# Kernel tuning notes

Hardware: AMD Instinct MI355X
Metric: run time of the kernel (lower is better)

The kernel has to match this reference:

```python
import jax, jax.numpy as jnp
import numpy as np

N = 100000   # subcomplex cells (nodes)
E = 600000   # edges in high-adjacency subcomplex graph
NB = 50000   # bridge (rank-0) cells
C = 128      # input_channels
H = 128      # hidden_channels
BN_EPS = 1e-5


def setup_inputs() -> dict:
    key = jax.random.key(0)
    ks = jax.random.split(key, 12)
    x = jax.random.normal(ks[0], (N, C), jnp.float32)
    x0 = jax.random.normal(ks[1], (NB, C), jnp.float32)
    edge_index = jax.random.randint(ks[2], (2, E), 0, N)
    bridge_index = jax.random.randint(ks[3], (E,), 0, NB)
    s1 = 1.0 / np.sqrt(C)
    s2 = 1.0 / np.sqrt(H)
    W1 = jax.random.uniform(ks[4], (C, H), jnp.float32, -s1, s1)
    b1 = jax.random.uniform(ks[5], (H,), jnp.float32, -s1, s1)
    W2 = jax.random.uniform(ks[6], (H, H), jnp.float32, -s2, s2)
    b2 = jax.random.uniform(ks[7], (H,), jnp.float32, -s2, s2)
    gamma1 = jnp.ones((H,), jnp.float32)
    beta1 = jnp.zeros((H,), jnp.float32)
    gamma2 = jnp.ones((H,), jnp.float32)
    beta2 = jnp.zeros((H,), jnp.float32)
    eps_gin = jnp.zeros((), jnp.float32)  # GIN train_eps, init 0
    return {"x": x, "x0": x0, "edge_index": edge_index, "bridge_index": bridge_index,
            "W1": W1, "b1": b1, "gamma1": gamma1, "beta1": beta1,
            "W2": W2, "b2": b2, "gamma2": gamma2, "beta2": beta2,
            "eps_gin": eps_gin}


def _bn(h, gamma, beta):
    # BatchNorm1d in training mode: batch stats over node dim, biased var
    mu = jnp.mean(h, axis=0)
    var = jnp.mean((h - mu) ** 2, axis=0)
    return gamma * (h - mu) * jax.lax.rsqrt(var + BN_EPS) + beta


def reference(x, x0, edge_index, bridge_index, W1, b1, gamma1, beta1,
              W2, b2, gamma2, beta2, eps_gin):
    src, dst = edge_index[0], edge_index[1]
    # edge attributes: gather bridge-cell features per edge  [E, C]
    edge_attr = x0[bridge_index]
    # GINE-style message: relu(x_j + e_ij), scatter-add into destination
    msg = jax.nn.relu(x[src] + edge_attr)
    aggr = jax.ops.segment_sum(msg, dst, num_segments=x.shape[0])  # [N, C]
    h = (1.0 + eps_gin) * x + aggr
    # 2-layer MLP: Linear -> BN -> ReLU, twice
    h = jax.nn.relu(_bn(h @ W1 + b1, gamma1, beta1))
    h = jax.nn.relu(_bn(h @ W2 + b2, gamma2, beta2))
    return h
```

## Files before the change

### kernel.cpp

```cpp
#include <hip/hip_runtime.h>


typedef __attribute__((ext_vector_type(8))) short bf16x8;
typedef __attribute__((ext_vector_type(4))) float floatx4;

__device__ __forceinline__ unsigned short f2bf(float f) {
  unsigned u = __float_as_uint(f);
  u += 0x7fff + ((u >> 16) & 1);
  return (unsigned short)(u >> 16);
}
__device__ __forceinline__ unsigned pk2(float a, float b) {
  return (unsigned)f2bf(a) | ((unsigned)f2bf(b) << 16);
}
__device__ __forceinline__ float bflo(unsigned u) { return __uint_as_float(u << 16); }
__device__ __forceinline__ float bfhi(unsigned u) { return __uint_as_float(u & 0xffff0000u); }

__global__ __launch_bounds__(256) void k_front(
    const float* __restrict__ x, const float* __restrict__ x0,
    const float* __restrict__ W1, const float* __restrict__ W2,
    unsigned short* __restrict__ WT1, unsigned short* __restrict__ WT2,
    uint4* __restrict__ zbase, int zitems, int zblocks,
    uint4* __restrict__ xb, int nx,
    uint4* __restrict__ x0b, int nx0) {
  int b = blockIdx.x;
  int tid = threadIdx.x;
  if (b < 2) {
    const float* W = b ? W2 : W1;
    unsigned short* WT = b ? WT2 : WT1;
#pragma unroll
    for (int i = 0; i < 16; ++i) {
      int g = tid + i * 256;
      int k = g >> 5;
      int n0 = (g & 31) * 4;
      float4 v = *(const float4*)(W + k * 128 + n0);
      WT[(n0 + 0) * 128 + k] = f2bf(v.x);
      WT[(n0 + 1) * 128 + k] = f2bf(v.y);
      WT[(n0 + 2) * 128 + k] = f2bf(v.z);
      WT[(n0 + 3) * 128 + k] = f2bf(v.w);
    }
    return;
  }
  if (b < 2 + zblocks) {
    int t = (b - 2) * 256 + tid;
    if (t < zitems) zbase[t] = make_uint4(0, 0, 0, 0);
    return;
  }
  int t = (b - 2 - zblocks) * 256 + tid;
  const float* s;
  uint4* d;
  if (t < nx) { s = x + (size_t)t * 8; d = xb + t; }
  else {
    t -= nx;
    if (t >= nx0) return;
    s = x0 + (size_t)t * 8; d = x0b + t;
  }
  float4 a = *(const float4*)s;
  float4 c = *(const float4*)(s + 4);
  uint4 o;
  o.x = pk2(a.x, a.y); o.y = pk2(a.z, a.w);
  o.z = pk2(c.x, c.y); o.w = pk2(c.z, c.w);
  *d = o;
}

__global__ __launch_bounds__(256) void k_scatter(
    const int* __restrict__ src, const int* __restrict__ dst,
    const int* __restrict__ bri, int* __restrict__ cnt,
    int2* __restrict__ slots, int E_) {
  int e = blockIdx.x * 256 + threadIdx.x;
  if (e >= E_) return;
  int d = dst[e];
  int pos = atomicAdd(&cnt[d], 1);
  if (pos < 32) slots[d * 32 + pos] = make_int2(src[e], bri[e]);
}

__device__ __forceinline__ void acc8(float* acc, uint4 xa, uint4 ea) {
  acc[0] += fmaxf(bflo(xa.x) + bflo(ea.x), 0.f);
  acc[1] += fmaxf(bfhi(xa.x) + bfhi(ea.x), 0.f);
  acc[2] += fmaxf(bflo(xa.y) + bflo(ea.y), 0.f);
  acc[3] += fmaxf(bfhi(xa.y) + bfhi(ea.y), 0.f);
  acc[4] += fmaxf(bflo(xa.z) + bflo(ea.z), 0.f);
  acc[5] += fmaxf(bfhi(xa.z) + bfhi(ea.z), 0.f);
  acc[6] += fmaxf(bflo(xa.w) + bflo(ea.w), 0.f);
  acc[7] += fmaxf(bfhi(xa.w) + bfhi(ea.w), 0.f);
}

__global__ __launch_bounds__(256) void k_aggr(
    const uint4* __restrict__ xb, const uint4* __restrict__ x0b,
    const int* __restrict__ cnt, const int2* __restrict__ slots,
    const float* __restrict__ eps, uint4* __restrict__ aggr, int n) {
  int tid = threadIdx.x;
  int node = blockIdx.x * 32 + (tid >> 3);
  if (node >= n) return;
  int q = (tid & 7) + blockIdx.y * 8;
  float s = 1.0f + eps[0];
  float acc[8];
  uint4 xi = xb[(size_t)node * 16 + q];
  acc[0] = s * bflo(xi.x); acc[1] = s * bfhi(xi.x);
  acc[2] = s * bflo(xi.y); acc[3] = s * bfhi(xi.y);
  acc[4] = s * bflo(xi.z); acc[5] = s * bfhi(xi.z);
  acc[6] = s * bflo(xi.w); acc[7] = s * bfhi(xi.w);
  int end = cnt[node];
  if (end > 32) end = 32;
  int base = node * 32;
  int j = 0;
  for (; j + 4 <= end; j += 4) {
    int4 pa = *(const int4*)(slots + base + j);
    int4 pb = *(const int4*)(slots + base + j + 2);
    uint4 xa0 = xb[(size_t)pa.x * 16 + q];
    uint4 ea0 = x0b[(size_t)pa.y * 16 + q];
    uint4 xa1 = xb[(size_t)pa.z * 16 + q];
    uint4 ea1 = x0b[(size_t)pa.w * 16 + q];
    uint4 xa2 = xb[(size_t)pb.x * 16 + q];
    uint4 ea2 = x0b[(size_t)pb.y * 16 + q];
    uint4 xa3 = xb[(size_t)pb.z * 16 + q];
    uint4 ea3 = x0b[(size_t)pb.w * 16 + q];
    acc8(acc, xa0, ea0);
    acc8(acc, xa1, ea1);
    acc8(acc, xa2, ea2);
    acc8(acc, xa3, ea3);
  }
  if (j + 2 <= end) {
    int4 pa = *(const int4*)(slots + base + j);
    uint4 xa0 = xb[(size_t)pa.x * 16 + q];
    uint4 ea0 = x0b[(size_t)pa.y * 16 + q];
    uint4 xa1 = xb[(size_t)pa.z * 16 + q];
    uint4 ea1 = x0b[(size_t)pa.w * 16 + q];
    acc8(acc, xa0, ea0);
    acc8(acc, xa1, ea1);
    j += 2;
  }
  if (j < end) {
    int2 p = slots[base + j];
    uint4 xa0 = xb[(size_t)p.x * 16 + q];
    uint4 ea0 = x0b[(size_t)p.y * 16 + q];
    acc8(acc, xa0, ea0);
  }
  uint4 o;
  o.x = pk2(acc[0], acc[1]); o.y = pk2(acc[2], acc[3]);
  o.z = pk2(acc[4], acc[5]); o.w = pk2(acc[6], acc[7]);
  aggr[(size_t)node * 16 + q] = o;
}

__global__ __launch_bounds__(256) void k_gemmb(
    const unsigned short* A, const unsigned short* __restrict__ WT,
    const float* __restrict__ bias,
    const float* __restrict__ psum, const float* __restrict__ psq,
    const float* __restrict__ gam, const float* __restrict__ bet,
    unsigned short* Out,
    float* __restrict__ part,
    int nrows, float inv_n, int fuse) {
  __shared__ unsigned short LDSraw[128 * 144];
  unsigned short* As = LDSraw;
  unsigned short* Bs = LDSraw + 128 * 72;
  __shared__ float sL[128], hL[128];
  __shared__ float redS[4][64], redQ[4][64];
  int tid = threadIdx.x;
  if (fuse && tid < 128) {
    float mu = psum[tid] * inv_n;
    float var = psq[tid] * inv_n - mu * mu;
    float rs = rsqrtf(var + 1e-5f);
    float sc = gam[tid] * rs;
    sL[tid] = sc;
    hL[tid] = bet[tid] - mu * sc;
  }
  __syncthreads();

  int row0 = blockIdx.x * 128;
  int lane = tid & 63;
  int wid = tid >> 6;
  int wr = (wid >> 1) * 64;
  int wc = (wid & 1) * 64;
  int lr = lane & 15;
  int quad = lane >> 4;

  floatx4 acc[4][4];
#pragma unroll
  for (int mi = 0; mi < 4; ++mi)
#pragma unroll
    for (int ni = 0; ni < 4; ++ni) acc[mi][ni] = (floatx4)0.0f;

  for (int kc = 0; kc < 128; kc += 64) {
    if (kc) __syncthreads();
#pragma unroll
    for (int i = 0; i < 4; ++i) {
      int g = tid + i * 256;
      int r = g >> 3;
      int c8 = g & 7;
      int row = row0 + r;
      uint4 v = make_uint4(0, 0, 0, 0);
      if (row < nrows)
        v = *(const uint4*)(A + (size_t)row * 128 + kc + c8 * 8);
      if (fuse) {
        int k = kc + c8 * 8;
        v.x = pk2(fmaxf(fmaf(sL[k + 0], bflo(v.x), hL[k + 0]), 0.f),
                  fmaxf(fmaf(sL[k + 1], bfhi(v.x), hL[k + 1]), 0.f));
        v.y = pk2(fmaxf(fmaf(sL[k + 2], bflo(v.y), hL[k + 2]), 0.f),
                  fmaxf(fmaf(sL[k + 3], bfhi(v.y), hL[k + 3]), 0.f));
        v.z = pk2(fmaxf(fmaf(sL[k + 4], bflo(v.z), hL[k + 4]), 0.f),
                  fmaxf(fmaf(sL[k + 5], bfhi(v.z), hL[k + 5]), 0.f));
        v.w = pk2(fmaxf(fmaf(sL[k + 6], bflo(v.w), hL[k + 6]), 0.f),
                  fmaxf(fmaf(sL[k + 7], bfhi(v.w), hL[k + 7]), 0.f));
      }
      *(uint4*)&As[r * 72 + c8 * 8] = v;
    }
#pragma unroll
    for (int i = 0; i < 4; ++i) {
      int g = tid + i * 256;
      int nn = g >> 3;
      int c8 = g & 7;
      *(uint4*)&Bs[nn * 72 + c8 * 8] =
          *(const uint4*)(WT + (size_t)nn * 128 + kc + c8 * 8);
    }
    __syncthreads();
#pragma unroll
    for (int ks = 0; ks < 2; ++ks) {
      int k0 = ks * 32 + quad * 8;
      bf16x8 af[4], bfr[4];
#pragma unroll
      for (int mi = 0; mi < 4; ++mi)
        af[mi] = *(const bf16x8*)&As[(wr + mi * 16 + lr) * 72 + k0];
#pragma unroll
      for (int ni = 0; ni < 4; ++ni)
        bfr[ni] = *(const bf16x8*)&Bs[(wc + ni * 16 + lr) * 72 + k0];
#pragma unroll
      for (int mi = 0; mi < 4; ++mi)
#pragma unroll
        for (int ni = 0; ni < 4; ++ni)
          acc[mi][ni] = __builtin_amdgcn_mfma_f32_16x16x32_bf16(
              af[mi], bfr[ni], acc[mi][ni], 0, 0, 0);
    }
  }
  __syncthreads();

  float bv[4];
#pragma unroll
  for (int ni = 0; ni < 4; ++ni) bv[ni] = bias[wc + ni * 16 + lr];
  float s_sum[4] = {0.f, 0.f, 0.f, 0.f};
  float s_sq[4]  = {0.f, 0.f, 0.f, 0.f};
#pragma unroll
  for (int mi = 0; mi < 4; ++mi) {
#pragma unroll
    for (int r = 0; r < 4; ++r) {
      int rl = wr + mi * 16 + quad * 4 + r;
      bool ok = (row0 + rl) < nrows;
#pragma unroll
      for (int ni = 0; ni < 4; ++ni) {
        int col = wc + ni * 16 + lr;
        float v = acc[mi][ni][r] + bv[ni];
        LDSraw[rl * 136 + col] = f2bf(v);
        if (ok) { s_sum[ni] += v; s_sq[ni] += v * v; }
      }
    }
  }
#pragma unroll
  for (int ni = 0; ni < 4; ++ni) {
    s_sum[ni] += __shfl_xor(s_sum[ni], 16, 64);
    s_sum[ni] += __shfl_xor(s_sum[ni], 32, 64);
    s_sq[ni]  += __shfl_xor(s_sq[ni], 16, 64);
    s_sq[ni]  += __shfl_xor(s_sq[ni], 32, 64);
  }
  if (quad == 0) {
#pragma unroll
    for (int ni = 0; ni < 4; ++ni) {
      redS[wid][ni * 16 + lr] = s_sum[ni];
      redQ[wid][ni * 16 + lr] = s_sq[ni];
    }
  }
  __syncthreads();
  if (tid < 128) {
    int half = tid >> 6;
    int cl = tid & 63;
    part[(size_t)blockIdx.x * 256 + tid] = redS[half][cl] + redS[half + 2][cl];
    part[(size_t)blockIdx.x * 256 + 128 + tid] = redQ[half][cl] + redQ[half + 2][cl];
  }
#pragma unroll
  for (int i = 0; i < 8; ++i) {
    int g = tid + i * 256;
    int r = g >> 4;
    int c8 = g & 15;
    if (row0 + r < nrows)
      *(uint4*)(Out + (size_t)(row0 + r) * 128 + c8 * 8) =
          *(const uint4*)&LDSraw[r * 136 + c8 * 8];
  }
}

__global__ __launch_bounds__(256) void k_red(
    const float* __restrict__ part, float* __restrict__ dst, int nb) {
  int c = threadIdx.x;
  int r0 = blockIdx.x * 32;
  int r1 = r0 + 32;
  if (r1 > nb) r1 = nb;
  float a = 0.f;
  for (int r = r0; r < r1; ++r) a += part[(size_t)r * 256 + c];
  unsafeAtomicAdd(&dst[c], a);
}

__global__ __launch_bounds__(256) void k_bnrelu(
    const uint4* __restrict__ h, const float* __restrict__ psum,
    const float* __restrict__ psq, const float* __restrict__ gam,
    const float* __restrict__ bet, float* __restrict__ out,
    int items, float inv_n) {
  __shared__ float sL[128], hL[128];
  int tid = threadIdx.x;
  if (tid < 128) {
    float mu = psum[tid] * inv_n;
    float var = psq[tid] * inv_n - mu * mu;
    float rs = rsqrtf(var + 1e-5f);
    float sc = gam[tid] * rs;
    sL[tid] = sc;
    hL[tid] = bet[tid] - mu * sc;
  }
  __syncthreads();
  int t = blockIdx.x * 256 + tid;
  if (t >= items) return;
  int c = (t & 15) * 8;
  uint4 v = h[t];
  float4 o1, o2;
  o1.x = fmaxf(fmaf(sL[c + 0], bflo(v.x), hL[c + 0]), 0.f);
  o1.y = fmaxf(fmaf(sL[c + 1], bfhi(v.x), hL[c + 1]), 0.f);
  o1.z = fmaxf(fmaf(sL[c + 2], bflo(v.y), hL[c + 2]), 0.f);
  o1.w = fmaxf(fmaf(sL[c + 3], bfhi(v.y), hL[c + 3]), 0.f);
  o2.x = fmaxf(fmaf(sL[c + 4], bflo(v.z), hL[c + 4]), 0.f);
  o2.y = fmaxf(fmaf(sL[c + 5], bfhi(v.z), hL[c + 5]), 0.f);
  o2.z = fmaxf(fmaf(sL[c + 6], bflo(v.w), hL[c + 6]), 0.f);
  o2.w = fmaxf(fmaf(sL[c + 7], bfhi(v.w), hL[c + 7]), 0.f);
  ((float4*)out)[(size_t)t * 2 + 0] = o1;
  ((float4*)out)[(size_t)t * 2 + 1] = o2;
}

extern "C" void kernel_launch(void* const* d_in, const int* in_sizes, int n_in,
                              void* d_out, int out_size, void* d_ws, size_t ws_size,
                              hipStream_t stream) {
  const float* x   = (const float*)d_in[0];
  const float* x0  = (const float*)d_in[1];
  const int*   ei  = (const int*)d_in[2];
  const int*   bi  = (const int*)d_in[3];
  const float* W1  = (const float*)d_in[4];
  const float* b1  = (const float*)d_in[5];
  const float* g1  = (const float*)d_in[6];
  const float* be1 = (const float*)d_in[7];
  const float* W2  = (const float*)d_in[8];
  const float* b2  = (const float*)d_in[9];
  const float* g2  = (const float*)d_in[10];
  const float* be2 = (const float*)d_in[11];
  const float* eps = (const float*)d_in[12];

  int N  = in_sizes[0] / 128;
  int NB = in_sizes[1] / 128;
  int E_ = in_sizes[3];
  const int* srcp = ei;
  const int* dstp = ei + E_;

  int2* slots = (int2*)d_ws;
  int* cnt    = (int*)(slots + (size_t)N * 32);
  float* stats = (float*)(cnt + N);
  float* sum1 = stats;
  float* sum2 = stats + 256;
  unsigned short* WT1  = (unsigned short*)(stats + 512);
  unsigned short* WT2  = WT1 + 16384;
  unsigned short* abuf = WT2 + 16384;

  unsigned short* xb  = (unsigned short*)d_out;
  unsigned short* x0b = xb + (size_t)N * 128;
  float* part = (float*)d_out;

  int zitems  = (N + 512 + 3) / 4;
  int zblocks = (zitems + 255) / 256;
  int nx  = N * 16;
  int nx0 = NB * 16;
  int cvtblocks = (nx + nx0 + 255) / 256;
  float inv_n = 1.0f / (float)N;

  k_front<<<2 + zblocks + cvtblocks, 256, 0, stream>>>(
      x, x0, W1, W2, WT1, WT2, (uint4*)cnt, zitems, zblocks,
      (uint4*)xb, nx, (uint4*)x0b, nx0);

  k_scatter<<<(E_ + 255) / 256, 256, 0, stream>>>(srcp, dstp, bi, cnt,
                                                  slots, E_);

  dim3 agrid((N * 8 + 255) / 256, 2);
  k_aggr<<<agrid, 256, 0, stream>>>(
      (const uint4*)xb, (const uint4*)x0b, cnt, slots, eps,
      (uint4*)abuf, N);

  int gblocks = (N + 127) / 128;
  int rblocks = (gblocks + 31) / 32;
  k_gemmb<<<gblocks, 256, 0, stream>>>(abuf, WT1, b1, nullptr, nullptr,
                                       nullptr, nullptr, abuf, part,
                                       N, inv_n, 0);
  k_red<<<rblocks, 256, 0, stream>>>(part, sum1, gblocks);
  k_gemmb<<<gblocks, 256, 0, stream>>>(abuf, WT2, b2, sum1, sum1 + 128,
                                       g1, be1, abuf, part, N, inv_n, 1);
  k_red<<<rblocks, 256, 0, stream>>>(part, sum2, gblocks);

  k_bnrelu<<<(N * 16 + 255) / 256, 256, 0, stream>>>(
      (const uint4*)abuf, sum2, sum2 + 128, g2, be2, (float*)d_out,
      N * 16, inv_n);
}
```

Measured before the change: 294.8 us.

## Fuse neighbor aggregation into first GEMM, building A tiles directly in LDS

The separate aggregation kernel is removed. The first GEMM now computes each 128-row aggregated tile itself, gathering neighbor and edge features into LDS one 64-column K-chunk at a time before running the MFMAs. This removes the write and re-read of the aggregated activation buffer and one kernel launch. The cost is a gather-heavy, latency-bound phase inside the GEMM kernel with fewer concurrent waves per row (only 256 threads per 128 rows, with `unroll 1`), which may hurt memory-level parallelism compared with the standalone aggregation grid. The partial-stats buffer is also moved so it no longer overlaps the bf16 copies of x and x0 that the fused kernel still reads.

```diff
diff --git a/kernel.cpp b/kernel.cpp
--- a/kernel.cpp
+++ b/kernel.cpp
@@ -84,17 +84,12 @@
   acc[7] += fmaxf(bfhi(xa.w) + bfhi(ea.w), 0.f);
 }
 
-__global__ __launch_bounds__(256) void k_aggr(
+__device__ __forceinline__ uint4 aggr_row(
     const uint4* __restrict__ xb, const uint4* __restrict__ x0b,
     const int* __restrict__ cnt, const int2* __restrict__ slots,
-    const float* __restrict__ eps, uint4* __restrict__ aggr, int n) {
-  int tid = threadIdx.x;
-  int node = blockIdx.x * 32 + (tid >> 3);
-  if (node >= n) return;
-  int q = (tid & 7) + blockIdx.y * 8;
-  float s = 1.0f + eps[0];
+    float s, int node, int qq) {
   float acc[8];
-  uint4 xi = xb[(size_t)node * 16 + q];
+  uint4 xi = xb[(size_t)node * 16 + qq];
   acc[0] = s * bflo(xi.x); acc[1] = s * bfhi(xi.x);
   acc[2] = s * bflo(xi.y); acc[3] = s * bfhi(xi.y);
   acc[4] = s * bflo(xi.z); acc[5] = s * bfhi(xi.z);
@@ -106,14 +101,14 @@
   for (; j + 4 <= end; j += 4) {
     int4 pa = *(const int4*)(slots + base + j);
     int4 pb = *(const int4*)(slots + base + j + 2);
-    uint4 xa0 = xb[(size_t)pa.x * 16 + q];
-    uint4 ea0 = x0b[(size_t)pa.y * 16 + q];
-    uint4 xa1 = xb[(size_t)pa.z * 16 + q];
-    uint4 ea1 = x0b[(size_t)pa.w * 16 + q];
-    uint4 xa2 = xb[(size_t)pb.x * 16 + q];
-    uint4 ea2 = x0b[(size_t)pb.y * 16 + q];
-    uint4 xa3 = xb[(size_t)pb.z * 16 + q];
-    uint4 ea3 = x0b[(size_t)pb.w * 16 + q];
+    uint4 xa0 = xb[(size_t)pa.x * 16 + qq];
+    uint4 ea0 = x0b[(size_t)pa.y * 16 + qq];
+    uint4 xa1 = xb[(size_t)pa.z * 16 + qq];
+    uint4 ea1 = x0b[(size_t)pa.w * 16 + qq];
+    uint4 xa2 = xb[(size_t)pb.x * 16 + qq];
+    uint4 ea2 = x0b[(size_t)pb.y * 16 + qq];
+    uint4 xa3 = xb[(size_t)pb.z * 16 + qq];
+    uint4 ea3 = x0b[(size_t)pb.w * 16 + qq];
     acc8(acc, xa0, ea0);
     acc8(acc, xa1, ea1);
     acc8(acc, xa2, ea2);
@@ -121,24 +116,138 @@
   }
   if (j + 2 <= end) {
     int4 pa = *(const int4*)(slots + base + j);
-    uint4 xa0 = xb[(size_t)pa.x * 16 + q];
-    uint4 ea0 = x0b[(size_t)pa.y * 16 + q];
-    uint4 xa1 = xb[(size_t)pa.z * 16 + q];
-    uint4 ea1 = x0b[(size_t)pa.w * 16 + q];
+    uint4 xa0 = xb[(size_t)pa.x * 16 + qq];
+    uint4 ea0 = x0b[(size_t)pa.y * 16 + qq];
+    uint4 xa1 = xb[(size_t)pa.z * 16 + qq];
+    uint4 ea1 = x0b[(size_t)pa.w * 16 + qq];
     acc8(acc, xa0, ea0);
     acc8(acc, xa1, ea1);
     j += 2;
   }
   if (j < end) {
     int2 p = slots[base + j];
-    uint4 xa0 = xb[(size_t)p.x * 16 + q];
-    uint4 ea0 = x0b[(size_t)p.y * 16 + q];
+    uint4 xa0 = xb[(size_t)p.x * 16 + qq];
+    uint4 ea0 = x0b[(size_t)p.y * 16 + qq];
     acc8(acc, xa0, ea0);
   }
   uint4 o;
   o.x = pk2(acc[0], acc[1]); o.y = pk2(acc[2], acc[3]);
   o.z = pk2(acc[4], acc[5]); o.w = pk2(acc[6], acc[7]);
-  aggr[(size_t)node * 16 + q] = o;
+  return o;
+}
+
+__global__ __launch_bounds__(256) void k_agemm(
+    const uint4* __restrict__ xb, const uint4* __restrict__ x0b,
+    const int* __restrict__ cnt, const int2* __restrict__ slots,
+    const float* __restrict__ eps,
+    const unsigned short* __restrict__ WT,
+    const float* __restrict__ bias,
+    unsigned short* __restrict__ Out,
+    float* __restrict__ part,
+    int nrows) {
+  __shared__ unsigned short LDSraw[128 * 144];
+  unsigned short* As = LDSraw;
+  __shared__ float redS[4][64], redQ[4][64];
+  int tid = threadIdx.x;
+  int row0 = blockIdx.x * 128;
+  int lane = tid & 63;
+  int wid = tid >> 6;
+  int wr = (wid >> 1) * 64;
+  int wc = (wid & 1) * 64;
+  int lr = lane & 15;
+  int quad = lane >> 4;
+  float s = 1.0f + eps[0];
+
+  floatx4 acc[4][4];
+#pragma unroll
+  for (int mi = 0; mi < 4; ++mi)
+#pragma unroll
+    for (int ni = 0; ni < 4; ++ni) acc[mi][ni] = (floatx4)0.0f;
+
+  for (int kc = 0; kc < 128; kc += 64) {
+    if (kc) __syncthreads();
+    int qq = (tid & 7) + (kc >> 3);
+#pragma unroll 1
+    for (int it = 0; it < 4; ++it) {
+      int r = it * 32 + (tid >> 3);
+      int node = row0 + r;
+      uint4 v = make_uint4(0, 0, 0, 0);
+      if (node < nrows)
+        v = aggr_row(xb, x0b, cnt, slots, s, node, qq);
+      *(uint4*)&As[r * 72 + (tid & 7) * 8] = v;
+    }
+    __syncthreads();
+#pragma unroll
+    for (int ks = 0; ks < 2; ++ks) {
+      int k0 = ks * 32 + quad * 8;
+      bf16x8 af[4], bfr[4];
+#pragma unroll
+      for (int mi = 0; mi < 4; ++mi)
+        af[mi] = *(const bf16x8*)&As[(wr + mi * 16 + lr) * 72 + k0];
+#pragma unroll
+      for (int ni = 0; ni < 4; ++ni)
+        bfr[ni] = *(const bf16x8*)(WT + (size_t)(wc + ni * 16 + lr) * 128 +
+                                   kc + k0);
+#pragma unroll
+      for (int mi = 0; mi < 4; ++mi)
+#pragma unroll
+        for (int ni = 0; ni < 4; ++ni)
+          acc[mi][ni] = __builtin_amdgcn_mfma_f32_16x16x32_bf16(
+              af[mi], bfr[ni], acc[mi][ni], 0, 0, 0);
+    }
+  }
+  __syncthreads();
+
+  float bv[4];
+#pragma unroll
+  for (int ni = 0; ni < 4; ++ni) bv[ni] = bias[wc + ni * 16 + lr];
+  float s_sum[4] = {0.f, 0.f, 0.f, 0.f};
+  float s_sq[4]  = {0.f, 0.f, 0.f, 0.f};
+#pragma unroll
+  for (int mi = 0; mi < 4; ++mi) {
+#pragma unroll
+    for (int r = 0; r < 4; ++r) {
+      int rl = wr + mi * 16 + quad * 4 + r;
+      bool ok = (row0 + rl) < nrows;
+#pragma unroll
+      for (int ni = 0; ni < 4; ++ni) {
+        int col = wc + ni * 16 + lr;
+        float v = acc[mi][ni][r] + bv[ni];
+        LDSraw[rl * 136 + col] = f2bf(v);
+        if (ok) { s_sum[ni] += v; s_sq[ni] += v * v; }
+      }
+    }
+  }
+#pragma unroll
+  for (int ni = 0; ni < 4; ++ni) {
+    s_sum[ni] += __shfl_xor(s_sum[ni], 16, 64);
+    s_sum[ni] += __shfl_xor(s_sum[ni], 32, 64);
+    s_sq[ni]  += __shfl_xor(s_sq[ni], 16, 64);
+    s_sq[ni]  += __shfl_xor(s_sq[ni], 32, 64);
+  }
+  if (quad == 0) {
+#pragma unroll
+    for (int ni = 0; ni < 4; ++ni) {
+      redS[wid][ni * 16 + lr] = s_sum[ni];
+      redQ[wid][ni * 16 + lr] = s_sq[ni];
+    }
+  }
+  __syncthreads();
+  if (tid < 128) {
+    int half = tid >> 6;
+    int cl = tid & 63;
+    part[(size_t)blockIdx.x * 256 + tid] = redS[half][cl] + redS[half + 2][cl];
+    part[(size_t)blockIdx.x * 256 + 128 + tid] = redQ[half][cl] + redQ[half + 2][cl];
+  }
+#pragma unroll
+  for (int i = 0; i < 8; ++i) {
+    int g = tid + i * 256;
+    int r = g >> 4;
+    int c8 = g & 15;
+    if (row0 + r < nrows)
+      *(uint4*)(Out + (size_t)(row0 + r) * 128 + c8 * 8) =
+          *(const uint4*)&LDSraw[r * 136 + c8 * 8];
+  }
 }
 
 __global__ __launch_bounds__(256) void k_gemmb(
@@ -362,7 +471,7 @@
 
   unsigned short* xb  = (unsigned short*)d_out;
   unsigned short* x0b = xb + (size_t)N * 128;
-  float* part = (float*)d_out;
+  float* part = (float*)((char*)d_out + (size_t)(N + NB) * 256);
 
   int zitems  = (N + 512 + 3) / 4;
   int zblocks = (zitems + 255) / 256;
@@ -378,16 +487,11 @@
   k_scatter<<<(E_ + 255) / 256, 256, 0, stream>>>(srcp, dstp, bi, cnt,
                                                   slots, E_);
 
-  dim3 agrid((N * 8 + 255) / 256, 2);
-  k_aggr<<<agrid, 256, 0, stream>>>(
-      (const uint4*)xb, (const uint4*)x0b, cnt, slots, eps,
-      (uint4*)abuf, N);
-
   int gblocks = (N + 127) / 128;
   int rblocks = (gblocks + 31) / 32;
-  k_gemmb<<<gblocks, 256, 0, stream>>>(abuf, WT1, b1, nullptr, nullptr,
-                                       nullptr, nullptr, abuf, part,
-                                       N, inv_n, 0);
+  k_agemm<<<gblocks, 256, 0, stream>>>(
+      (const uint4*)xb, (const uint4*)x0b, cnt, slots, eps, WT1, b1,
+      abuf, part, N);
   k_red<<<rblocks, 256, 0, stream>>>(part, sum1, gblocks);
   k_gemmb<<<gblocks, 256, 0, stream>>>(abuf, WT2, b2, sum1, sum1 + 128,
                                        g1, be1, abuf, part, N, inv_n, 1);
```

After: 320.7 us. 1.09x slower.

## Merge convert, scatter and aggregate into one cooperative kernel with grid syncs

Applied to the files above, without the earlier changes.

Replaces the three launches (bf16 conversion with zeroing, edge scatter into slots, neighbor aggregation) with a single cooperative kernel. It uses grid-stride loops and grid-wide barriers between phases, and falls back to three per-phase launches if the cooperative launch is unavailable. The goal is to cut kernel launch gaps and tail effects between the preprocessing stages. In exchange, the grid is capped at 2048 blocks, which may lower parallelism in the gather phase, and grid.sync adds barrier cost.

```diff
diff --git a/kernel.cpp b/kernel.cpp
--- a/kernel.cpp
+++ b/kernel.cpp
@@ -1,4 +1,7 @@
 #include <hip/hip_runtime.h>
+#include <hip/hip_cooperative_groups.h>
+
+namespace cg = cooperative_groups;
 
 
 typedef __attribute__((ext_vector_type(8))) short bf16x8;
@@ -15,63 +18,17 @@
 __device__ __forceinline__ float bflo(unsigned u) { return __uint_as_float(u << 16); }
 __device__ __forceinline__ float bfhi(unsigned u) { return __uint_as_float(u & 0xffff0000u); }
 
-__global__ __launch_bounds__(256) void k_front(
-    const float* __restrict__ x, const float* __restrict__ x0,
-    const float* __restrict__ W1, const float* __restrict__ W2,
-    unsigned short* __restrict__ WT1, unsigned short* __restrict__ WT2,
-    uint4* __restrict__ zbase, int zitems, int zblocks,
-    uint4* __restrict__ xb, int nx,
-    uint4* __restrict__ x0b, int nx0) {
-  int b = blockIdx.x;
-  int tid = threadIdx.x;
-  if (b < 2) {
-    const float* W = b ? W2 : W1;
-    unsigned short* WT = b ? WT2 : WT1;
-#pragma unroll
-    for (int i = 0; i < 16; ++i) {
-      int g = tid + i * 256;
-      int k = g >> 5;
-      int n0 = (g & 31) * 4;
-      float4 v = *(const float4*)(W + k * 128 + n0);
-      WT[(n0 + 0) * 128 + k] = f2bf(v.x);
-      WT[(n0 + 1) * 128 + k] = f2bf(v.y);
-      WT[(n0 + 2) * 128 + k] = f2bf(v.z);
-      WT[(n0 + 3) * 128 + k] = f2bf(v.w);
-    }
-    return;
-  }
-  if (b < 2 + zblocks) {
-    int t = (b - 2) * 256 + tid;
-    if (t < zitems) zbase[t] = make_uint4(0, 0, 0, 0);
-    return;
-  }
-  int t = (b - 2 - zblocks) * 256 + tid;
-  const float* s;
-  uint4* d;
-  if (t < nx) { s = x + (size_t)t * 8; d = xb + t; }
-  else {
-    t -= nx;
-    if (t >= nx0) return;
-    s = x0 + (size_t)t * 8; d = x0b + t;
-  }
-  float4 a = *(const float4*)s;
-  float4 c = *(const float4*)(s + 4);
-  uint4 o;
-  o.x = pk2(a.x, a.y); o.y = pk2(a.z, a.w);
-  o.z = pk2(c.x, c.y); o.w = pk2(c.z, c.w);
-  *d = o;
-}
-
-__global__ __launch_bounds__(256) void k_scatter(
-    const int* __restrict__ src, const int* __restrict__ dst,
-    const int* __restrict__ bri, int* __restrict__ cnt,
-    int2* __restrict__ slots, int E_) {
-  int e = blockIdx.x * 256 + threadIdx.x;
-  if (e >= E_) return;
-  int d = dst[e];
-  int pos = atomicAdd(&cnt[d], 1);
-  if (pos < 32) slots[d * 32 + pos] = make_int2(src[e], bri[e]);
-}
+struct PreParams {
+  const float* x; const float* x0;
+  const int* src; const int* dst; const int* bri;
+  const float* eps;
+  int2* slots; int* cnt;
+  const float* W1; const float* W2;
+  unsigned short* WT1; unsigned short* WT2;
+  unsigned short* abuf;
+  float* dout;
+  int N; int NB; int E;
+};
 
 __device__ __forceinline__ void acc8(float* acc, uint4 xa, uint4 ea) {
   acc[0] += fmaxf(bflo(xa.x) + bflo(ea.x), 0.f);
@@ -84,17 +41,12 @@
   acc[7] += fmaxf(bfhi(xa.w) + bfhi(ea.w), 0.f);
 }
 
-__global__ __launch_bounds__(256) void k_aggr(
+__device__ __forceinline__ uint4 aggr_row(
     const uint4* __restrict__ xb, const uint4* __restrict__ x0b,
     const int* __restrict__ cnt, const int2* __restrict__ slots,
-    const float* __restrict__ eps, uint4* __restrict__ aggr, int n) {
-  int tid = threadIdx.x;
-  int node = blockIdx.x * 32 + (tid >> 3);
-  if (node >= n) return;
-  int q = (tid & 7) + blockIdx.y * 8;
-  float s = 1.0f + eps[0];
+    float s, int node, int qq) {
   float acc[8];
-  uint4 xi = xb[(size_t)node * 16 + q];
+  uint4 xi = xb[(size_t)node * 16 + qq];
   acc[0] = s * bflo(xi.x); acc[1] = s * bfhi(xi.x);
   acc[2] = s * bflo(xi.y); acc[3] = s * bfhi(xi.y);
   acc[4] = s * bflo(xi.z); acc[5] = s * bfhi(xi.z);
@@ -106,14 +58,14 @@
   for (; j + 4 <= end; j += 4) {
     int4 pa = *(const int4*)(slots + base + j);
     int4 pb = *(const int4*)(slots + base + j + 2);
-    uint4 xa0 = xb[(size_t)pa.x * 16 + q];
-    uint4 ea0 = x0b[(size_t)pa.y * 16 + q];
-    uint4 xa1 = xb[(size_t)pa.z * 16 + q];
-    uint4 ea1 = x0b[(size_t)pa.w * 16 + q];
-    uint4 xa2 = xb[(size_t)pb.x * 16 + q];
-    uint4 ea2 = x0b[(size_t)pb.y * 16 + q];
-    uint4 xa3 = xb[(size_t)pb.z * 16 + q];
-    uint4 ea3 = x0b[(size_t)pb.w * 16 + q];
+    uint4 xa0 = xb[(size_t)pa.x * 16 + qq];
+    uint4 ea0 = x0b[(size_t)pa.y * 16 + qq];
+    uint4 xa1 = xb[(size_t)pa.z * 16 + qq];
+    uint4 ea1 = x0b[(size_t)pa.w * 16 + qq];
+    uint4 xa2 = xb[(size_t)pb.x * 16 + qq];
+    uint4 ea2 = x0b[(size_t)pb.y * 16 + qq];
+    uint4 xa3 = xb[(size_t)pb.z * 16 + qq];
+    uint4 ea3 = x0b[(size_t)pb.w * 16 + qq];
     acc8(acc, xa0, ea0);
     acc8(acc, xa1, ea1);
     acc8(acc, xa2, ea2);
@@ -121,24 +73,97 @@
   }
   if (j + 2 <= end) {
     int4 pa = *(const int4*)(slots + base + j);
-    uint4 xa0 = xb[(size_t)pa.x * 16 + q];
-    uint4 ea0 = x0b[(size_t)pa.y * 16 + q];
-    uint4 xa1 = xb[(size_t)pa.z * 16 + q];
-    uint4 ea1 = x0b[(size_t)pa.w * 16 + q];
+    uint4 xa0 = xb[(size_t)pa.x * 16 + qq];
+    uint4 ea0 = x0b[(size_t)pa.y * 16 + qq];
+    uint4 xa1 = xb[(size_t)pa.z * 16 + qq];
+    uint4 ea1 = x0b[(size_t)pa.w * 16 + qq];
     acc8(acc, xa0, ea0);
     acc8(acc, xa1, ea1);
     j += 2;
   }
   if (j < end) {
-    int2 p = slots[base + j];
-    uint4 xa0 = xb[(size_t)p.x * 16 + q];
-    uint4 ea0 = x0b[(size_t)p.y * 16 + q];
+    int2 pp = slots[base + j];
+    uint4 xa0 = xb[(size_t)pp.x * 16 + qq];
+    uint4 ea0 = x0b[(size_t)pp.y * 16 + qq];
     acc8(acc, xa0, ea0);
   }
   uint4 o;
   o.x = pk2(acc[0], acc[1]); o.y = pk2(acc[2], acc[3]);
   o.z = pk2(acc[4], acc[5]); o.w = pk2(acc[6], acc[7]);
-  aggr[(size_t)node * 16 + q] = o;
+  return o;
+}
+
+__device__ __forceinline__ void run_pre(const PreParams& p, int phase) {
+  int tid = threadIdx.x;
+  int nb = gridDim.x;
+  int gt0 = blockIdx.x * 256 + tid;
+  int gstride = nb * 256;
+  uint4* xbv  = (uint4*)p.dout;
+  uint4* x0bv = xbv + (size_t)p.N * 16;
+  int nx = p.N * 16, nx0 = p.NB * 16;
+
+  if (phase == 0) {
+    int zitems = (p.N + 512 + 3) >> 2;
+    for (int t = gt0; t < zitems; t += gstride)
+      ((uint4*)p.cnt)[t] = make_uint4(0, 0, 0, 0);
+    for (int t = gt0; t < 8192; t += gstride) {
+      int w = t >> 12;
+      int g = t & 4095;
+      const float* W = w ? p.W2 : p.W1;
+      unsigned short* WT = w ? p.WT2 : p.WT1;
+      int k = g >> 5;
+      int n0 = (g & 31) * 4;
+      float4 v = *(const float4*)(W + k * 128 + n0);
+      WT[(n0 + 0) * 128 + k] = f2bf(v.x);
+      WT[(n0 + 1) * 128 + k] = f2bf(v.y);
+      WT[(n0 + 2) * 128 + k] = f2bf(v.z);
+      WT[(n0 + 3) * 128 + k] = f2bf(v.w);
+    }
+    for (int t = gt0; t < nx + nx0; t += gstride) {
+      const float* sp;
+      uint4* dp;
+      if (t < nx) { sp = p.x + (size_t)t * 8; dp = xbv + t; }
+      else { sp = p.x0 + (size_t)(t - nx) * 8; dp = x0bv + (t - nx); }
+      float4 a = *(const float4*)sp;
+      float4 c4 = *(const float4*)(sp + 4);
+      uint4 o;
+      o.x = pk2(a.x, a.y); o.y = pk2(a.z, a.w);
+      o.z = pk2(c4.x, c4.y); o.w = pk2(c4.z, c4.w);
+      *dp = o;
+    }
+  } else if (phase == 1) {
+    for (int e = gt0; e < p.E; e += gstride) {
+      int d = p.dst[e];
+      int pos = atomicAdd(&p.cnt[d], 1);
+      if (pos < 32) p.slots[d * 32 + pos] = make_int2(p.src[e], p.bri[e]);
+    }
+  } else {
+    float s = 1.0f + p.eps[0];
+    int nAb = (p.N * 8 + 255) / 256;
+    for (int t = blockIdx.x; t < 2 * nAb; t += nb) {
+      int by = (t >= nAb) ? 1 : 0;
+      int bx = t - by * nAb;
+      int node = bx * 32 + (tid >> 3);
+      if (node < p.N) {
+        int qq = (tid & 7) + by * 8;
+        uint4 o = aggr_row(xbv, x0bv, p.cnt, p.slots, s, node, qq);
+        ((uint4*)p.abuf)[(size_t)node * 16 + qq] = o;
+      }
+    }
+  }
+}
+
+__global__ __launch_bounds__(256) void k_pre(PreParams p) {
+  cg::grid_group grid = cg::this_grid();
+  run_pre(p, 0);
+  __threadfence(); grid.sync();
+  run_pre(p, 1);
+  __threadfence(); grid.sync();
+  run_pre(p, 2);
+}
+
+__global__ __launch_bounds__(256) void k_prephase(PreParams p, int phase) {
+  run_pre(p, phase);
 }
 
 __global__ __launch_bounds__(256) void k_gemmb(
@@ -331,25 +356,10 @@
 extern "C" void kernel_launch(void* const* d_in, const int* in_sizes, int n_in,
                               void* d_out, int out_size, void* d_ws, size_t ws_size,
                               hipStream_t stream) {
-  const float* x   = (const float*)d_in[0];
-  const float* x0  = (const float*)d_in[1];
-  const int*   ei  = (const int*)d_in[2];
-  const int*   bi  = (const int*)d_in[3];
-  const float* W1  = (const float*)d_in[4];
-  const float* b1  = (const float*)d_in[5];
-  const float* g1  = (const float*)d_in[6];
-  const float* be1 = (const float*)d_in[7];
-  const float* W2  = (const float*)d_in[8];
-  const float* b2  = (const float*)d_in[9];
-  const float* g2  = (const float*)d_in[10];
-  const float* be2 = (const float*)d_in[11];
-  const float* eps = (const float*)d_in[12];
-
   int N  = in_sizes[0] / 128;
   int NB = in_sizes[1] / 128;
   int E_ = in_sizes[3];
-  const int* srcp = ei;
-  const int* dstp = ei + E_;
+  const int* ei = (const int*)d_in[2];
 
   int2* slots = (int2*)d_ws;
   int* cnt    = (int*)(slots + (size_t)N * 32);
@@ -360,31 +370,59 @@
   unsigned short* WT2  = WT1 + 16384;
   unsigned short* abuf = WT2 + 16384;
 
-  unsigned short* xb  = (unsigned short*)d_out;
-  unsigned short* x0b = xb + (size_t)N * 128;
+  PreParams p;
+  p.x   = (const float*)d_in[0];
+  p.x0  = (const float*)d_in[1];
+  p.src = ei;
+  p.dst = ei + E_;
+  p.bri = (const int*)d_in[3];
+  p.eps = (const float*)d_in[12];
+  p.slots = slots; p.cnt = cnt;
+  p.W1 = (const float*)d_in[4];
+  p.W2 = (const float*)d_in[8];
+  p.WT1 = WT1; p.WT2 = WT2; p.abuf = abuf;
+  p.dout = (float*)d_out;
+  p.N = N; p.NB = NB; p.E = E_;
+
+  const float* b1  = (const float*)d_in[5];
+  const float* g1  = (const float*)d_in[6];
+  const float* be1 = (const float*)d_in[7];
+  const float* b2  = (const float*)d_in[9];
+  const float* g2  = (const float*)d_in[10];
+  const float* be2 = (const float*)d_in[11];
   float* part = (float*)d_out;
 
-  int zitems  = (N + 512 + 3) / 4;
-  int zblocks = (zitems + 255) / 256;
-  int nx  = N * 16;
-  int nx0 = NB * 16;
-  int cvtblocks = (nx + nx0 + 255) / 256;
-  float inv_n = 1.0f / (float)N;
-
-  k_front<<<2 + zblocks + cvtblocks, 256, 0, stream>>>(
-      x, x0, W1, W2, WT1, WT2, (uint4*)cnt, zitems, zblocks,
-      (uint4*)xb, nx, (uint4*)x0b, nx0);
-
-  k_scatter<<<(E_ + 255) / 256, 256, 0, stream>>>(srcp, dstp, bi, cnt,
-                                                  slots, E_);
-
-  dim3 agrid((N * 8 + 255) / 256, 2);
-  k_aggr<<<agrid, 256, 0, stream>>>(
-      (const uint4*)xb, (const uint4*)x0b, cnt, slots, eps,
-      (uint4*)abuf, N);
+  static int coop_grid = -2;
+  if (coop_grid == -2) {
+    int nbcu = 0;
+    hipError_t e = hipOccupancyMaxActiveBlocksPerMultiprocessor(
+        &nbcu, (const void*)k_pre, 256, 0);
+    if (e == hipSuccess && nbcu >= 1) {
+      long g = (long)nbcu * 256;
+      coop_grid = (int)(g > 2048 ? 2048 : g);
+      if (coop_grid < 256) coop_grid = -1;
+    } else {
+      coop_grid = -1;
+    }
+  }
+
+  bool pre_done = false;
+  if (coop_grid > 0) {
+    void* args[] = {(void*)&p};
+    hipError_t e = hipLaunchCooperativeKernel(
+        (const void*)k_pre, dim3(coop_grid), dim3(256), args, 0, stream);
+    if (e == hipSuccess) pre_done = true;
+    else coop_grid = -1;
+  }
+  if (!pre_done) {
+    k_prephase<<<2048, 256, 0, stream>>>(p, 0);
+    k_prephase<<<2048, 256, 0, stream>>>(p, 1);
+    k_prephase<<<3125, 256, 0, stream>>>(p, 2);
+  }
 
   int gblocks = (N + 127) / 128;
   int rblocks = (gblocks + 31) / 32;
+  float inv_n = 1.0f / (float)N;
   k_gemmb<<<gblocks, 256, 0, stream>>>(abuf, WT1, b1, nullptr, nullptr,
                                        nullptr, nullptr, abuf, part,
                                        N, inv_n, 0);
```

Result: slower. 591.0 us (+100.5%).
